# Kernel tuning notes

Measured on AMD Instinct MI355X. Metric: run time of the kernel, lower is better.

Reference implementation:

```python
import jax, jax.numpy as jnp
import numpy as np

W = 8          # block window width
R = 4          # block stride (upsampling ratio)
STRICT_CAUSAL = False
EPS = 1e-8


def _triangular_kernel(w_len: int) -> jnp.ndarray:
    # matches torch: up=linspace(0,1,W//2+1); w=cat(up[:-1], flip(up)) -> length W+1 for even W
    up = jnp.linspace(0.0, 1.0, w_len // 2 + 1)
    w = jnp.concatenate([up[:-1], up[::-1]])
    if w.shape[0] < w_len:  # static pad (only for odd W edge cases)
        w = jnp.concatenate([w, jnp.full((w_len - w.shape[0],), w[-1])])
    return w


def _overlap_matrix(S: int, N: int, kernel: jnp.ndarray, dtype) -> jnp.ndarray:
    # A[t, i] = kernel[t - i*R] if 0 <= t - i*R <= W-1 (band), then row-normalized.
    t = jnp.arange(S)[:, None]              # [S,1]
    s = jnp.arange(N)[None, :] * R          # [1,N] block starts
    off = t - s                             # [S,N]
    valid = (off >= 0) & (off <= W - 1)
    if STRICT_CAUSAL:
        valid = valid & (t >= s + W - 1)    # only t >= block end
    vals = kernel[jnp.clip(off, 0, W - 1)].astype(dtype)
    A = jnp.where(valid, vals, jnp.zeros((), dtype))
    A = A / (A.sum(axis=1, keepdims=True) + EPS)
    return A


def setup_inputs() -> dict:
    key = jax.random.key(0)
    B, N, H = 4, 2048, 1024
    Z = jax.random.normal(key, (B, N, H), dtype=jnp.float32)
    return {"Z": Z, "S_out": 8192}


def reference(Z, S_out):
    B, N, H = Z.shape
    kernel = _triangular_kernel(W)
    A = _overlap_matrix(S_out, N, kernel, Z.dtype)   # [S,N] banded, row-normalized
    return jnp.einsum('sn,bnh->bsh', A, Z)           # [B,S,H]
```

## Files before the change

kernel.cpp:

```cpp
#include <hip/hip_runtime.h>


typedef float f4 __attribute__((ext_vector_type(4)));

#define B_DIM 4
#define N_DIM 2048
#define H4    256
#define S_DIM 8192
#define NBLK  (B_DIM * (N_DIM / 2))
#define NXCD  8
#define CHUNK (NBLK / NXCD)

__global__ __launch_bounds__(256)
void Upscaler_33294586479031_kernel(const f4* __restrict__ Z,
                                    f4* __restrict__ out) {
    const int bid = blockIdx.x;
    const int swz = (bid & (NXCD - 1)) * CHUNK + (bid >> 3);

    const int q2 = swz & (N_DIM / 2 - 1);
    const int b  = swz >> 10;
    const int h  = threadIdx.x;
    const int q0 = q2 * 2;

    const f4* zbase = Z + (size_t)b * (N_DIM * H4) + h;

    const int qm = (q0 > 0) ? (q0 - 1) : 0;
    const f4 zm = zbase[(size_t)qm * H4];
    const f4 z0 = zbase[(size_t)q0 * H4];
    const f4 z1 = zbase[(size_t)(q0 + 1) * H4];

    f4* ob = out + (size_t)b * (S_DIM * H4) + (size_t)(4 * q0) * H4 + h;

    if (q0 == 0) {
        const f4 zero = (f4)(0.0f);
        __builtin_nontemporal_store(zero, &ob[0 * H4]);
        __builtin_nontemporal_store(z0,   &ob[1 * H4]);
        __builtin_nontemporal_store(z0,   &ob[2 * H4]);
        __builtin_nontemporal_store(z0,   &ob[3 * H4]);
    } else {
        #pragma unroll
        for (int m = 0; m < 4; ++m) {
            const float w1 = 0.25f * (float)m;
            const float w0 = 1.0f - w1;
            const f4 r = w0 * zm + w1 * z0;
            __builtin_nontemporal_store(r, &ob[m * H4]);
        }
    }

    #pragma unroll
    for (int m = 0; m < 4; ++m) {
        const float w1 = 0.25f * (float)m;
        const float w0 = 1.0f - w1;
        const f4 r = w0 * z0 + w1 * z1;
        __builtin_nontemporal_store(r, &ob[(4 + m) * H4]);
    }
}

extern "C" void kernel_launch(void* const* d_in, const int* in_sizes, int n_in,
                              void* d_out, int out_size, void* d_ws, size_t ws_size,
                              hipStream_t stream) {
    const f4* Z = (const f4*)d_in[0];
    f4* out     = (f4*)d_out;

    Upscaler_33294586479031_kernel<<<NBLK, 256, 0, stream>>>(Z, out);
}
```

Before: 165.7 us.

## Process four input rows per block and drop XCD swizzle and nontemporal stores

Each block now handles four consecutive input rows instead of two, so the halo row read per block is amortised over more outputs and the grid shrinks to a quarter of the blocks in the original two-row scheme. The XCD-aware block index swizzle is removed in favour of a linear mapping. Stores are changed from nontemporal builtins to plain stores, which may change how the write stream interacts with the caches. Fewer blocks reduce parallelism and may affect how well the memory-bound write traffic is spread.

```diff
diff --git a/kernel.cpp b/kernel.cpp
--- a/kernel.cpp
+++ b/kernel.cpp
@@ -7,52 +7,52 @@
 #define N_DIM 2048
 #define H4    256
 #define S_DIM 8192
-#define NBLK  (B_DIM * (N_DIM / 2))
-#define NXCD  8
-#define CHUNK (NBLK / NXCD)
+#define LQ    4
+#define NBLK  (B_DIM * (N_DIM / LQ))
 
 __global__ __launch_bounds__(256)
 void Upscaler_33294586479031_kernel(const f4* __restrict__ Z,
                                     f4* __restrict__ out) {
     const int bid = blockIdx.x;
-    const int swz = (bid & (NXCD - 1)) * CHUNK + (bid >> 3);
-
-    const int q2 = swz & (N_DIM / 2 - 1);
-    const int b  = swz >> 10;
-    const int h  = threadIdx.x;
-    const int q0 = q2 * 2;
+    const int b   = bid >> 9;
+    const int qs  = (bid & 511) * LQ;
+    const int h   = threadIdx.x;
 
     const f4* zbase = Z + (size_t)b * (N_DIM * H4) + h;
+    f4* ob = out + (size_t)b * (S_DIM * H4) + (size_t)(4 * qs) * H4 + h;
 
-    const int qm = (q0 > 0) ? (q0 - 1) : 0;
-    const f4 zm = zbase[(size_t)qm * H4];
-    const f4 z0 = zbase[(size_t)q0 * H4];
-    const f4 z1 = zbase[(size_t)(q0 + 1) * H4];
-
-    f4* ob = out + (size_t)b * (S_DIM * H4) + (size_t)(4 * q0) * H4 + h;
-
-    if (q0 == 0) {
+    if (qs == 0) {
+        f4 zp = zbase[0];
         const f4 zero = (f4)(0.0f);
-        __builtin_nontemporal_store(zero, &ob[0 * H4]);
-        __builtin_nontemporal_store(z0,   &ob[1 * H4]);
-        __builtin_nontemporal_store(z0,   &ob[2 * H4]);
-        __builtin_nontemporal_store(z0,   &ob[3 * H4]);
+        ob[0 * H4] = zero;
+        ob[1 * H4] = zp;
+        ob[2 * H4] = zp;
+        ob[3 * H4] = zp;
+        ob += 4 * H4;
+        #pragma unroll
+        for (int i = 1; i < LQ; ++i) {
+            const f4 zc = zbase[(size_t)i * H4];
+            #pragma unroll
+            for (int m = 0; m < 4; ++m) {
+                const float w1 = 0.25f * (float)m;
+                ob[m * H4] = (1.0f - w1) * zp + w1 * zc;
+            }
+            zp = zc;
+            ob += 4 * H4;
+        }
     } else {
+        f4 zp = zbase[(size_t)(qs - 1) * H4];
         #pragma unroll
-        for (int m = 0; m < 4; ++m) {
-            const float w1 = 0.25f * (float)m;
-            const float w0 = 1.0f - w1;
-            const f4 r = w0 * zm + w1 * z0;
-            __builtin_nontemporal_store(r, &ob[m * H4]);
+        for (int i = 0; i < LQ; ++i) {
+            const f4 zc = zbase[(size_t)(qs + i) * H4];
+            #pragma unroll
+            for (int m = 0; m < 4; ++m) {
+                const float w1 = 0.25f * (float)m;
+                ob[m * H4] = (1.0f - w1) * zp + w1 * zc;
+            }
+            zp = zc;
+            ob += 4 * H4;
         }
-    }
-
-    #pragma unroll
-    for (int m = 0; m < 4; ++m) {
-        const float w1 = 0.25f * (float)m;
-        const float w0 = 1.0f - w1;
-        const f4 r = w0 * z0 + w1 * z1;
-        __builtin_nontemporal_store(r, &ob[(4 + m) * H4]);
     }
 }
 
```

Result: faster. 157.3 us (-5.1%).
